# Optimization experiments

Hardware: AMD Instinct MI355X
Metric: run time of the kernel (lower is better)

The kernel has to match this reference:

```python
import jax, jax.numpy as jnp
import numpy as np

START_IDX = 1  # PAD_IDX = 0, END_IDX = 2 (unused in teacher-forcing path)
B, N, F = 16, 49, 1024
H, E, V = 1024, 1024, 15000
S, W = 5, 12


def setup_inputs() -> dict:
    key = jax.random.key(0)
    ks = jax.random.split(key, 16)
    def w(k, shape, s=0.02):
        return jax.random.normal(k, shape, dtype=jnp.float32) * s
    emb = w(ks[0], (V, E)).at[0].set(0.0)  # padding_idx = 0
    return dict(
        features=jax.random.normal(ks[1], (B, N, F), dtype=jnp.float32),
        reports=jax.random.randint(ks[2], (B, S, W), 0, V),
        attn_w1=w(ks[3], (F + H, H)), attn_b1=jnp.zeros((H,), jnp.float32),
        attn_w2=w(ks[4], (H, 1)), attn_b2=jnp.zeros((1,), jnp.float32),
        s_wih=w(ks[5], (4 * H, F)), s_whh=w(ks[6], (4 * H, H)),
        s_bih=jnp.zeros((4 * H,), jnp.float32), s_bhh=jnp.zeros((4 * H,), jnp.float32),
        stop_w=w(ks[7], (H, 1)), stop_b=jnp.zeros((1,), jnp.float32),
        emb=emb,
        w_wih=w(ks[8], (4 * H, E)), w_whh=w(ks[9], (4 * H, H)),
        w_bih=jnp.zeros((4 * H,), jnp.float32), w_bhh=jnp.zeros((4 * H,), jnp.float32),
        fc_w=w(ks[10], (H, V)), fc_b=jnp.zeros((V,), jnp.float32),
    )


def _lstm_cell(x, h, c, wih, whh, bih, bhh):
    # PyTorch LSTMCell: gates ordered i, f, g, o
    gates = x @ wih.T + h @ whh.T + (bih + bhh)
    i, f, g, o = jnp.split(gates, 4, axis=-1)
    c = jax.nn.sigmoid(f) * c + jax.nn.sigmoid(i) * jnp.tanh(g)
    h = jax.nn.sigmoid(o) * jnp.tanh(c)
    return h, c


def _attention(features, h, w1, b1, w2, b2):
    # features [B,N,F], h [B,H] -> additive 2-layer attention over N locations
    b, n, _ = features.shape
    hcat = jnp.broadcast_to(h[:, None, :], (b, n, h.shape[-1]))
    x = jnp.concatenate([features, hcat], axis=-1)           # [B,N,F+H]
    e = (jnp.tanh(x @ w1 + b1) @ w2 + b2)[..., 0]            # [B,N]
    scores = jax.nn.softmax(e, axis=-1)
    att = jnp.einsum('bn,bnf->bf', scores, features)          # [B,F]
    return att, scores


def _forward(features, reports, attn_w1, attn_b1, attn_w2, attn_b2,
             s_wih, s_whh, s_bih, s_bhh, stop_w, stop_b, emb,
             w_wih, w_whh, w_bih, w_bhh, fc_w, fc_b):
    bsz = features.shape[0]
    h0 = jnp.zeros((bsz, s_whh.shape[-1]), features.dtype)
    att0, _ = _attention(features, h0, attn_w1, attn_b1, attn_w2, attn_b2)
    start_emb = jnp.broadcast_to(emb[START_IDX][None, :], (bsz, emb.shape[-1]))

    def sentence_step(carry, reports_i):   # reports_i: [W, B] teacher-forcing tokens
        h, c, att = carry
        h, c = _lstm_cell(att, h, c, s_wih, s_whh, s_bih, s_bhh)
        czero = jnp.zeros_like(h)

        def word_step(wc, idx):
            hw, cw, inp = wc
            hw, cw = _lstm_cell(inp, hw, cw, w_wih, w_whh, w_bih, w_bhh)
            pred = hw @ fc_w + fc_b                           # [B,V]
            return (hw, cw, emb[idx]), pred

        # word LSTM initialized with h=topic, c=0; first input = <start> embedding
        _, preds = jax.lax.scan(word_step, (h, czero, start_emb), reports_i)  # [W,B,V]
        stop = jax.nn.sigmoid(h @ stop_w + stop_b)[:, 0]      # [B]
        att, scores = _attention(features, h, attn_w1, attn_b1, attn_w2, attn_b2)
        return (h, c, att), (preds, stop, scores)

    reports_sw = jnp.transpose(reports, (1, 2, 0))            # [S,W,B]
    _, (seq, stops, scores) = jax.lax.scan(sentence_step, (h0, h0, att0), reports_sw)
    seq_out = jnp.transpose(seq, (2, 0, 1, 3))                # [B,S,W,V]
    stops_out = jnp.transpose(stops, (1, 0))                  # [B,S]
    scores_out = jnp.transpose(scores, (1, 0, 2))             # [B,S,N]
    return seq_out, stops_out, scores_out


def reference(features, reports, attn_w1, attn_b1, attn_w2, attn_b2,
              s_wih, s_whh, s_bih, s_bhh, stop_w, stop_b, emb,
              w_wih, w_whh, w_bih, w_bhh, fc_w, fc_b):
    return _forward(features, reports, attn_w1, attn_b1, attn_w2, attn_b2,
                    s_wih, s_whh, s_bih, s_bhh, stop_w, stop_b, emb,
                    w_wih, w_whh, w_bih, w_bhh, fc_w, fc_b)
```

## Files before the change

kernel.cpp:

```cpp
#include <hip/hip_runtime.h>
#include <hip/hip_bf16.h>

#define B_  16
#define S_  5
#define W_  12
#define NL_ 49
#define H_  1024
#define V_  15000
#define SEQ_N   14400000
#define STOP_N  80
#define OUT_STOP (SEQ_N)
#define OUT_SCORE (SEQ_N + STOP_N)

typedef __attribute__((ext_vector_type(8))) short     short8;
typedef __attribute__((ext_vector_type(4))) float     f32x4;
typedef __attribute__((ext_vector_type(4))) unsigned int u32x4;
typedef __attribute__((ext_vector_type(4))) unsigned short us4;

#define OFF_FCWT   0ull
#define OFF_WWHHP  30720000ull
#define OFF_WWIHP  39108608ull
#define OFF_WSCATP 47497216ull
#define OFF_W1AT   64274432ull
#define OFF_W1BT   66371584ull
#define OFF_FBF    68468736ull
#define OFF_XIN    70074368ull
#define OFF_PF     72040448ull
#define OFF_XW     75251712ull
#define OFF_HBALL  90980352ull
#define OFF_HWBF0  92946432ull
#define OFF_HWBF1  93110272ull
#define OFF_ACAT1  93274112ull
#define OFF_H      93339648ull
#define OFF_EVAL   93405184ull
#define OFF_ACAT0  93408384ull
#define OFF_C      93473920ull
#define OFF_CW     93539456ull
#define OFF_HPROJ  93867136ull
#define WS_TOTAL   93932672ull
#define ZERO_BASE  OFF_ACAT0
#define ZERO_BYTES (524288ull)

__device__ __forceinline__ unsigned short f2bf(float x){
  unsigned u = __float_as_uint(x);
  u += 0x7fffu + ((u >> 16) & 1u);
  return (unsigned short)(u >> 16);
}
__device__ __forceinline__ float sigm(float x){ return 1.f/(1.f+expf(-x)); }

typedef __attribute__((address_space(3))) unsigned int  as3_u32;
typedef __attribute__((address_space(1))) const unsigned int as1_u32;

__device__ __forceinline__ void gl16(const void* g, void* l){
  __builtin_amdgcn_global_load_lds((as1_u32*)g, (as3_u32*)l, 16, 0, 0);
}

template<int ROWS,int CH,int NW>
__device__ __forceinline__ void stage_swz(const unsigned short* __restrict__ gbase, int grs,
                                          unsigned short* lds, int wid, int lane,
                                          int r0, int rmax){
  constexpr int RPI = 64/CH;
  constexpr int NISS = ROWS/RPI;
  const int r_in = lane / CH;
  const int cbp  = lane % CH;
  #pragma unroll
  for (int it = wid; it < NISS; it += NW){
    int rl = it*RPI + r_in;
    int gr = r0 + rl; gr = gr < rmax ? gr : rmax-1;
    int cb = cbp ^ (rl & 7);
    gl16(gbase + (size_t)gr*grs + cb*8, lds + it*RPI*CH*8);
  }
}

__device__ __forceinline__ void transp64(const float* __restrict__ src, int sld,
                                         int rb, int cb, int Cc,
                                         unsigned short* __restrict__ dst, int dld,
                                         float (*t)[65])
{
  const int tx = threadIdx.x & 15, ty = threadIdx.x >> 4;
  #pragma unroll
  for (int ii = 0; ii < 4; ii++){
    int r = ty + ii*16;
    int c = cb + tx*4;
    const float* s = src + (size_t)(rb + r)*sld + c;
    f32x4 v;
    if (c + 4 <= Cc) v = *(const f32x4*)s;
    else {
      v[0] = (c   < Cc) ? s[0] : 0.f;
      v[1] = (c+1 < Cc) ? s[1] : 0.f;
      v[2] = (c+2 < Cc) ? s[2] : 0.f;
      v[3] = (c+3 < Cc) ? s[3] : 0.f;
    }
    t[r][tx*4+0]=v[0]; t[r][tx*4+1]=v[1]; t[r][tx*4+2]=v[2]; t[r][tx*4+3]=v[3];
  }
  __syncthreads();
  #pragma unroll
  for (int ii = 0; ii < 4; ii++){
    int c = ty + ii*16;
    if (cb + c < Cc){
      int r4 = tx*4;
      us4 o; o[0]=f2bf(t[r4][c]); o[1]=f2bf(t[r4+1][c]); o[2]=f2bf(t[r4+2][c]); o[3]=f2bf(t[r4+3][c]);
      *(us4*)(dst + (size_t)(cb + c)*dld + rb + r4) = o;
    }
  }
}

#define U0 200704u
#define U1 (U0+1048576u)
#define U2 (U1+1048576u)
#define U3 (U2+1048576u)
#define U4 (U3+1048576u)
#define U5 (U4+245760u)
#define NCVT_BLK 1280
#define NTR_BLK  2136
#define NZ_BLK   16
#define NPREP    (NCVT_BLK + NTR_BLK + NZ_BLK)

__device__ __forceinline__ void cvt_gate_unit(const float* __restrict__ src,
                                              unsigned short* __restrict__ dst,
                                              unsigned e, int dld, int doff){
  int n = e >> 8, cc = (e & 255)*4;
  int gate = (n >> 4) & 3, j = ((n >> 6) << 4) | (n & 15);
  f32x4 v = *(const f32x4*)(src + ((size_t)(gate*1024 + j) << 10) + cc);
  us4 o; o[0]=f2bf(v[0]); o[1]=f2bf(v[1]); o[2]=f2bf(v[2]); o[3]=f2bf(v[3]);
  *(us4*)(dst + (size_t)n*dld + doff + cc) = o;
}

__global__ void k_prep(const float* __restrict__ features,
                       const float* __restrict__ w_whh, const float* __restrict__ w_wih,
                       const float* __restrict__ s_wih, const float* __restrict__ s_whh,
                       const float* __restrict__ emb, const int* __restrict__ reports,
                       const float* __restrict__ attn_w1, const float* __restrict__ fc_w,
                       unsigned short* __restrict__ FBF, unsigned short* __restrict__ WWHHP,
                       unsigned short* __restrict__ WWIHP, unsigned short* __restrict__ WSCATP,
                       unsigned short* __restrict__ XIN,
                       unsigned short* __restrict__ W1AT, unsigned short* __restrict__ W1BT,
                       unsigned short* __restrict__ FCWT, char* __restrict__ zbase)
{
  __shared__ float t[64][65];
  int bx = blockIdx.x;
  if (bx < NCVT_BLK){
    for (unsigned u = bx*256u + threadIdx.x; u < U5; u += NCVT_BLK*256u){
      if (u < U0){
        int idx = u*4;
        f32x4 v = *(const f32x4*)(features + idx);
        us4 o; o[0]=f2bf(v[0]); o[1]=f2bf(v[1]); o[2]=f2bf(v[2]); o[3]=f2bf(v[3]);
        *(us4*)(FBF + idx) = o;
      } else if (u < U1){
        cvt_gate_unit(w_whh, WWHHP, u - U0, 1024, 0);
      } else if (u < U2){
        cvt_gate_unit(w_wih, WWIHP, u - U1, 1024, 0);
      } else if (u < U3){
        cvt_gate_unit(s_wih, WSCATP, u - U2, 2048, 0);
      } else if (u < U4){
        cvt_gate_unit(s_whh, WSCATP, u - U3, 2048, 1024);
      } else {
        unsigned e = u - U4;
        int m = e >> 8, k = (e & 255)*4;
        int w = m / 80, r = m % 80, s = r >> 4, b = r & 15;
        int tok = (w == 0) ? 1 : reports[b*60 + s*12 + (w-1)];
        f32x4 v = *(const f32x4*)(emb + ((size_t)tok << 10) + k);
        us4 o; o[0]=f2bf(v[0]); o[1]=f2bf(v[1]); o[2]=f2bf(v[2]); o[3]=f2bf(v[3]);
        *(us4*)(XIN + (size_t)m*1024 + k) = o;
      }
    }
  } else if (bx < NCVT_BLK + NTR_BLK){
    int base = (bx - NCVT_BLK)*2;
    #pragma unroll
    for (int bt = 0; bt < 2; bt++){
      if (bt) __syncthreads();
      int tile = base + bt;
      if (tile < 512){
        int z = tile >> 8, rem = tile & 255;
        int rb = (rem & 15)*64, cb = (rem >> 4)*64;
        transp64(attn_w1 + (size_t)z*1024*1024, 1024, rb, cb, 1024, z ? W1BT : W1AT, 1024, t);
      } else {
        int ft = tile - 512;
        int rb = (ft & 15)*64, cb = (ft >> 4)*64;
        transp64(fc_w, V_, rb, cb, V_, FCWT, 1024, t);
      }
    }
  } else {
    int idx = bx - (NCVT_BLK + NTR_BLK);
    #pragma unroll
    for (int it = 0; it < 8; it++){
      size_t off = ((size_t)(idx + it*NZ_BLK))*4096 + threadIdx.x*16;
      *(u32x4*)(zbase + off) = (u32x4){0u,0u,0u,0u};
    }
  }
}

template<int BM,int BN,int BK,int WM,int WN,int EPI>
__device__ __forceinline__ void gemm_core(
    unsigned short* As, unsigned short* Bs,
    const unsigned short* __restrict__ A, int lda,
    const unsigned short* __restrict__ Bt, int ldb,
    float* __restrict__ C, int ldc,
    const float* __restrict__ bias,
    int M, int N, int K, int n0, int m0)
{
  constexpr int NWV = WM*WN;
  constexpr int CH = BK/8;
  const int tid  = threadIdx.x;
  const int lane = tid & 63;
  const int wave = tid >> 6;
  constexpr int WROWS = BM/WM, WCOLS = BN/WN;
  constexpr int FM = WROWS/16, FN = WCOLS/16;
  const int wm = wave / WN, wn = wave % WN;
  const int g = lane >> 4, fr = lane & 15;
  const int sx = fr & 7;

  f32x4 acc[FM][FN];
  #pragma unroll
  for (int a=0;a<FM;a++)
    #pragma unroll
    for (int b=0;b<FN;b++) acc[a][b] = (f32x4){0.f,0.f,0.f,0.f};

  for (int k0 = 0; k0 < K; k0 += BK) {
    if (k0) __syncthreads();
    stage_swz<BM,CH,NWV>(A + k0, lda, As, wave, lane, m0, M);
    stage_swz<BN,CH,NWV>(Bt + k0, ldb, Bs, wave, lane, n0, N);
    __syncthreads();
    #pragma unroll
    for (int kk = 0; kk < BK; kk += 32) {
      const int so = ((kk/8 + g) ^ sx) * 8;
      short8 af[FM], bt[FN];
      #pragma unroll
      for (int fm=0; fm<FM; fm++)
        af[fm] = *(const short8*)(As + (wm*WROWS + fm*16 + fr)*BK + so);
      #pragma unroll
      for (int fn=0; fn<FN; fn++)
        bt[fn] = *(const short8*)(Bs + (wn*WCOLS + fn*16 + fr)*BK + so);
      #pragma unroll
      for (int fm=0; fm<FM; fm++)
        #pragma unroll
        for (int fn=0; fn<FN; fn++)
          acc[fm][fn] = __builtin_amdgcn_mfma_f32_16x16x32_bf16(af[fm], bt[fn], acc[fm][fn], 0, 0, 0);
    }
  }

  #pragma unroll
  for (int fm=0; fm<FM; fm++)
    #pragma unroll
    for (int fn=0; fn<FN; fn++)
      #pragma unroll
      for (int j=0; j<4; j++){
        int m = m0 + wm*WROWS + fm*16 + g*4 + j;
        int n = n0 + wn*WCOLS + fn*16 + fr;
        if (m < M && n < N) {
          float v = acc[fm][fn][j];
          if (EPI == 1 || EPI == 2) v += bias[n];
          if (EPI == 2) {
            int b = m & 15, s = (m >> 4) % 5, w = m / 80;
            __builtin_nontemporal_store(v, &C[(size_t)((b*5 + s)*12 + w)*V_ + n]);
          } else if (EPI == 3) {
            __builtin_nontemporal_store(v, &C[(size_t)m*ldc + n]);
          } else {
            C[(size_t)m*ldc + n] = v;
          }
        }
      }
}

template<int BM,int BN,int BK,int WM,int WN,int EPI>
__global__ void k_gemm(const unsigned short* __restrict__ A, int lda,
                       const unsigned short* __restrict__ Bt, int ldb,
                       float* __restrict__ C, int ldc,
                       const float* __restrict__ bias,
                       int M, int N, int K)
{
  __shared__ __align__(16) unsigned short As[BM*BK];
  __shared__ __align__(16) unsigned short Bs[BN*BK];
  const int n0 = blockIdx.x * BN, m0 = blockIdx.y * BM;
  if (n0 >= N) return;
  gemm_core<BM,BN,BK,WM,WN,EPI>(As, Bs, A, lda, Bt, ldb, C, ldc, bias, M, N, K, n0, m0);
}

__global__ void __launch_bounds__(256) k_pf_xw(
    const unsigned short* __restrict__ FBF, const unsigned short* __restrict__ W1AT,
    float* __restrict__ PF, const float* __restrict__ attn_b1,
    const unsigned short* __restrict__ XIN, const unsigned short* __restrict__ WWIHP,
    float* __restrict__ XW)
{
  extern __shared__ __align__(16) unsigned short smem[];
  unsigned short* As = smem;
  unsigned short* Bs = smem + 64*128;
  int bx = blockIdx.x;
  if (bx < 208){
    int n0 = (bx & 15)*64, m0 = (bx >> 4)*64;
    gemm_core<64,64,128,2,2,1>(As, Bs, FBF,1024, W1AT,1024, PF,1024, attn_b1,
                               784,1024,1024, n0, m0);
  } else {
    int t = bx - 208;
    int n0 = (t & 31)*128, m0 = (t >> 5)*64;
    gemm_core<64,128,128,2,2,3>(As, Bs, XIN,1024, WWIHP,1024, XW,4096, nullptr,
                                960,4096,1024, n0, m0);
  }
}

template<int BM,int BN,int BK,int WN,int SENT>
__global__ void k_gemm_cell(const unsigned short* __restrict__ A, int lda,
                            const unsigned short* __restrict__ Bt, int ldb,
                            const float* __restrict__ Xg, int ldx,
                            const float* __restrict__ bih, const float* __restrict__ bhh,
                            float* __restrict__ cst,
                            unsigned short* __restrict__ h1, int ldh1,
                            unsigned short* __restrict__ h2,
                            float* __restrict__ hf,
                            int M, int K)
{
  constexpr int CH = BK/8;
  __shared__ __align__(16) unsigned short As[BM*BK];
  __shared__ __align__(16) unsigned short Bs[BN*BK];
  const int tid  = threadIdx.x;
  const int lane = tid & 63;
  const int wn   = tid >> 6;
  const int n0 = blockIdx.x * BN, m0 = blockIdx.y * BM;
  const int g = lane >> 4, fr = lane & 15;
  const int sx = fr & 7;

  f32x4 acc[4];
  #pragma unroll
  for (int b=0;b<4;b++) acc[b] = (f32x4){0.f,0.f,0.f,0.f};

  for (int k0 = 0; k0 < K; k0 += BK) {
    if (k0) __syncthreads();
    stage_swz<BM,CH,WN>(A + k0, lda, As, wn, lane, m0, M);
    stage_swz<BN,CH,WN>(Bt + k0, ldb, Bs, wn, lane, n0, 4096);
    __syncthreads();
    #pragma unroll
    for (int kk = 0; kk < BK; kk += 32) {
      const int so = ((kk/8 + g) ^ sx) * 8;
      short8 af = *(const short8*)(As + fr*BK + so);
      #pragma unroll
      for (int fn=0; fn<4; fn++){
        short8 bt = *(const short8*)(Bs + (wn*64 + fn*16 + fr)*BK + so);
        acc[fn] = __builtin_amdgcn_mfma_f32_16x16x32_bf16(af, bt, acc[fn], 0, 0, 0);
      }
    }
  }

  const int nb = n0 + wn*64 + fr;
  const int j  = ((n0 + wn*64) >> 2) + fr;
  const float b0 = bih[j]        + bhh[j];
  const float b1 = bih[1024 + j] + bhh[1024 + j];
  const float b2 = bih[2048 + j] + bhh[2048 + j];
  const float b3 = bih[3072 + j] + bhh[3072 + j];
  #pragma unroll
  for (int jj=0; jj<4; jj++){
    int m = m0 + g*4 + jj;
    if (m < M){
      float gi = acc[0][jj] + b0;
      float gf = acc[1][jj] + b1;
      float gg = acc[2][jj] + b2;
      float go = acc[3][jj] + b3;
      if (!SENT){
        const float* xg = Xg + (size_t)m*ldx + nb;
        gi += xg[0]; gf += xg[16]; gg += xg[32]; go += xg[48];
      }
      float cn = sigm(gf)*cst[m*1024 + j] + sigm(gi)*tanhf(gg);
      float hn = sigm(go)*tanhf(cn);
      cst[m*1024 + j] = cn;
      unsigned short hb = f2bf(hn);
      h1[(size_t)m*ldh1 + j] = hb;
      h2[(size_t)m*1024 + j] = hb;
      if (SENT) hf[m*1024 + j] = hn;
    }
  }
}

__global__ void k_attn_e(const float* __restrict__ PF, const float* __restrict__ hproj,
                         const float* __restrict__ w2, float* __restrict__ evals)
{
  const int bn = blockIdx.x;
  const int b  = bn / NL_;
  const int tid = threadIdx.x;
  __shared__ float red[4];
  const float* pf = PF + ((size_t)bn << 10);
  const float* hp = hproj + (b << 10);
  int k = tid * 4;
  f32x4 a = *(const f32x4*)(pf + k);
  f32x4 hh = *(const f32x4*)(hp + k);
  f32x4 w = *(const f32x4*)(w2 + k);
  float p = tanhf(a[0]+hh[0])*w[0] + tanhf(a[1]+hh[1])*w[1]
          + tanhf(a[2]+hh[2])*w[2] + tanhf(a[3]+hh[3])*w[3];
  #pragma unroll
  for (int o = 32; o; o >>= 1) p += __shfl_down(p, o, 64);
  if ((tid & 63) == 0) red[tid >> 6] = p;
  __syncthreads();
  if (tid == 0) evals[bn] = red[0] + red[1] + red[2] + red[3];
}

template<int INIT>
__global__ void k_attn_fin(const float* __restrict__ evals, const float* __restrict__ features,
                           const float* __restrict__ h, const float* __restrict__ stop_w,
                           const float* __restrict__ stop_b,
                           unsigned short* __restrict__ Acat, float* __restrict__ outp, int s)
{
  const int b = blockIdx.x, tid = threadIdx.x;
  __shared__ float scs[64];
  __shared__ float red[4];
  if (tid < 64){
    float e = (tid < NL_) ? evals[b*NL_ + tid] : -1e30f;
    float mx = e;
    #pragma unroll
    for (int o = 32; o; o >>= 1) mx = fmaxf(mx, __shfl_xor(mx, o, 64));
    float ex = (tid < NL_) ? expf(e - mx) : 0.f;
    float dn = ex;
    #pragma unroll
    for (int o = 32; o; o >>= 1) dn += __shfl_xor(dn, o, 64);
    float sc = ex / dn;
    if (tid < NL_){
      scs[tid] = sc;
      if (!INIT) outp[OUT_SCORE + (b*5 + s)*NL_ + tid] = sc;
    }
  }
  __syncthreads();
  {
    int f0 = tid * 4;
    f32x4 a = (f32x4){0.f,0.f,0.f,0.f};
    const float* fb = features + (((size_t)b*NL_) << 10) + f0;
    #pragma unroll 7
    for (int n = 0; n < NL_; n++){
      f32x4 v = *(const f32x4*)(fb + ((size_t)n << 10));
      float sc = scs[n];
      a[0] += sc*v[0]; a[1] += sc*v[1]; a[2] += sc*v[2]; a[3] += sc*v[3];
    }
    us4 o4; o4[0]=f2bf(a[0]); o4[1]=f2bf(a[1]); o4[2]=f2bf(a[2]); o4[3]=f2bf(a[3]);
    *(us4*)(Acat + b*2048 + f0) = o4;
  }
  if (!INIT){
    int k = tid * 4;
    f32x4 hv = *(const f32x4*)(h + (b << 10) + k);
    f32x4 sw = *(const f32x4*)(stop_w + k);
    float p = hv[0]*sw[0] + hv[1]*sw[1] + hv[2]*sw[2] + hv[3]*sw[3];
    #pragma unroll
    for (int o = 32; o; o >>= 1) p += __shfl_down(p, o, 64);
    if ((tid & 63) == 0) red[tid >> 6] = p;
    __syncthreads();
    if (tid == 0) outp[OUT_STOP + b*5 + s] = sigm(red[0]+red[1]+red[2]+red[3] + stop_b[0]);
  }
}

extern "C" void kernel_launch(void* const* d_in, const int* in_sizes, int n_in,
                              void* d_out, int out_size, void* d_ws, size_t ws_size,
                              hipStream_t stream)
{
  const float* features = (const float*)d_in[0];
  const int*   reports  = (const int*)d_in[1];
  const float* attn_w1  = (const float*)d_in[2];
  const float* attn_b1  = (const float*)d_in[3];
  const float* attn_w2  = (const float*)d_in[4];
  const float* s_wih    = (const float*)d_in[6];
  const float* s_whh    = (const float*)d_in[7];
  const float* s_bih    = (const float*)d_in[8];
  const float* s_bhh    = (const float*)d_in[9];
  const float* stop_w   = (const float*)d_in[10];
  const float* stop_b   = (const float*)d_in[11];
  const float* emb      = (const float*)d_in[12];
  const float* w_wih    = (const float*)d_in[13];
  const float* w_whh    = (const float*)d_in[14];
  const float* w_bih    = (const float*)d_in[15];
  const float* w_bhh    = (const float*)d_in[16];
  const float* fc_w     = (const float*)d_in[17];
  const float* fc_b     = (const float*)d_in[18];
  float* out = (float*)d_out;
  char*  ws  = (char*)d_ws;
  if (ws_size < WS_TOTAL) return;

  unsigned short* FCWT   = (unsigned short*)(ws + OFF_FCWT);
  unsigned short* WWHHP  = (unsigned short*)(ws + OFF_WWHHP);
  unsigned short* WWIHP  = (unsigned short*)(ws + OFF_WWIHP);
  unsigned short* WSCATP = (unsigned short*)(ws + OFF_WSCATP);
  unsigned short* W1AT   = (unsigned short*)(ws + OFF_W1AT);
  unsigned short* W1BT   = (unsigned short*)(ws + OFF_W1BT);
  unsigned short* FBF    = (unsigned short*)(ws + OFF_FBF);
  unsigned short* XIN    = (unsigned short*)(ws + OFF_XIN);
  float*          PF     = (float*)(ws + OFF_PF);
  float*          XW     = (float*)(ws + OFF_XW);
  unsigned short* HBALL  = (unsigned short*)(ws + OFF_HBALL);
  unsigned short* HW0    = (unsigned short*)(ws + OFF_HWBF0);
  unsigned short* HW1    = (unsigned short*)(ws + OFF_HWBF1);
  unsigned short* ACAT0  = (unsigned short*)(ws + OFF_ACAT0);
  unsigned short* ACAT1  = (unsigned short*)(ws + OFF_ACAT1);
  float*          Hst    = (float*)(ws + OFF_H);
  float*          Cst    = (float*)(ws + OFF_C);
  float*          CW     = (float*)(ws + OFF_CW);
  float*          HPROJ  = (float*)(ws + OFF_HPROJ);
  float*          EVAL   = (float*)(ws + OFF_EVAL);

  k_prep<<<NPREP, 256, 0, stream>>>(features, w_whh, w_wih, s_wih, s_whh, emb, reports,
                                    attn_w1, fc_w,
                                    FBF, WWHHP, WWIHP, WSCATP, XIN, W1AT, W1BT, FCWT,
                                    ws + ZERO_BASE);

  k_pf_xw<<<688, 256, 49152, stream>>>(FBF, W1AT, PF, attn_b1, XIN, WWIHP, XW);

  k_attn_e<<<784, 256, 0, stream>>>(PF, HPROJ, attn_w2, EVAL);
  k_attn_fin<1><<<16, 256, 0, stream>>>(EVAL, features, Hst, stop_w, stop_b, ACAT0, out, 0);

  unsigned short* ACS[2] = {ACAT0, ACAT1};
  for (int s = 0; s < S_; s++){
    unsigned short* cur = ACS[s & 1];
    unsigned short* nxt = ACS[(s + 1) & 1];
    k_gemm_cell<16,128,256,2,1><<<dim3(32,1), 128, 0, stream>>>(
        cur, 2048, WSCATP, 2048, nullptr, 0, s_bih, s_bhh, Cst,
        nxt + 1024, 2048, HW0 + s*16*1024, Hst, 16, 2048);
    k_gemm<16,64,256,1,4,0><<<dim3(16,1), 256, 0, stream>>>(
        nxt + 1024, 2048, W1BT, 1024, HPROJ, 1024, nullptr, 16, 1024, 1024);
    k_attn_e<<<784, 256, 0, stream>>>(PF, HPROJ, attn_w2, EVAL);
    k_attn_fin<0><<<16, 256, 0, stream>>>(EVAL, features, Hst, stop_w, stop_b, nxt, out, s);
  }

  unsigned short* HW[2] = {HW0, HW1};
  for (int w = 0; w < W_; w++){
    k_gemm_cell<16,128,256,2,0><<<dim3(32,5), 128, 0, stream>>>(
        HW[w & 1], 1024, WWHHP, 1024, XW + (size_t)w*80*4096, 4096, w_bih, w_bhh, CW,
        HW[(w + 1) & 1], 1024, HBALL + (size_t)w*80*1024, nullptr, 80, 1024);
  }

  k_gemm<64,128,64,2,2,2><<<dim3(120,15), 256, 0, stream>>>(HBALL,1024, FCWT,1024, out,V_, fc_b, 960,15000,1024);
}
```

Baseline: 504.0 us.

## Fuse word-LSTM time steps into one persistent kernel with grid barrier

Replaces twelve separate per-step word-LSTM GEMM+cell launches with a single persistent kernel of 160 blocks that loops over time steps and synchronizes through a global atomic counter barrier in workspace. The barrier memory is zeroed by the prep kernel. This is meant to remove per-launch overhead and inter-kernel gaps along the serial recurrence. It relies on all 160 blocks being co-resident and adds spin-wait latency on each step.

Result: slower. 621.7 us (+23.4%).

```diff
diff --git a/kernel.cpp b/kernel.cpp
--- a/kernel.cpp
+++ b/kernel.cpp
@@ -37,9 +37,9 @@
 #define OFF_C      93473920ull
 #define OFF_CW     93539456ull
 #define OFF_HPROJ  93867136ull
-#define WS_TOTAL   93932672ull
+#define OFF_BAR    93932672ull
+#define WS_TOTAL   93936768ull
 #define ZERO_BASE  OFF_ACAT0
-#define ZERO_BYTES (524288ull)
 
 __device__ __forceinline__ unsigned short f2bf(float x){
   unsigned u = __float_as_uint(x);
@@ -187,6 +187,8 @@
       size_t off = ((size_t)(idx + it*NZ_BLK))*4096 + threadIdx.x*16;
       *(u32x4*)(zbase + off) = (u32x4){0u,0u,0u,0u};
     }
+    if (idx == 0)
+      *(u32x4*)(zbase + 524288 + threadIdx.x*16) = (u32x4){0u,0u,0u,0u};
   }
 }
 
@@ -365,6 +367,87 @@
       h1[(size_t)m*ldh1 + j] = hb;
       h2[(size_t)m*1024 + j] = hb;
       if (SENT) hf[m*1024 + j] = hn;
+    }
+  }
+}
+
+__global__ void __launch_bounds__(128) k_word_chain(
+    const unsigned short* __restrict__ Bt,
+    const float* __restrict__ XW,
+    const float* __restrict__ bih, const float* __restrict__ bhh,
+    float* __restrict__ cw,
+    unsigned short* __restrict__ HW0, unsigned short* __restrict__ HW1,
+    unsigned short* __restrict__ Hball,
+    unsigned* __restrict__ bar)
+{
+  constexpr int BK = 256, CH = BK/8;
+  __shared__ __align__(16) unsigned short As[16*BK];
+  __shared__ __align__(16) unsigned short Bs[128*BK];
+  const int tid = threadIdx.x, lane = tid & 63, wn = tid >> 6;
+  const int n0 = blockIdx.x * 128, m0 = blockIdx.y * 16;
+  const int g = lane >> 4, fr = lane & 15, sx = fr & 7;
+
+  const int nb = n0 + wn*64 + fr;
+  const int j  = ((n0 + wn*64) >> 2) + fr;
+  const float b0 = bih[j]        + bhh[j];
+  const float b1 = bih[1024 + j] + bhh[1024 + j];
+  const float b2 = bih[2048 + j] + bhh[2048 + j];
+  const float b3 = bih[3072 + j] + bhh[3072 + j];
+  unsigned short* HW[2] = {HW0, HW1};
+
+  for (int w = 0; w < W_; w++){
+    const unsigned short* A = HW[w & 1];
+    f32x4 acc[4];
+    #pragma unroll
+    for (int b=0;b<4;b++) acc[b] = (f32x4){0.f,0.f,0.f,0.f};
+    for (int k0 = 0; k0 < 1024; k0 += BK){
+      if (k0) __syncthreads();
+      stage_swz<16,CH,2>(A + k0, 1024, As, wn, lane, m0, 80);
+      stage_swz<128,CH,2>(Bt + k0, 1024, Bs, wn, lane, n0, 4096);
+      __syncthreads();
+      #pragma unroll
+      for (int kk = 0; kk < BK; kk += 32){
+        const int so = ((kk/8 + g) ^ sx) * 8;
+        short8 af = *(const short8*)(As + fr*BK + so);
+        #pragma unroll
+        for (int fn=0; fn<4; fn++){
+          short8 bt = *(const short8*)(Bs + (wn*64 + fn*16 + fr)*BK + so);
+          acc[fn] = __builtin_amdgcn_mfma_f32_16x16x32_bf16(af, bt, acc[fn], 0, 0, 0);
+        }
+      }
+    }
+    unsigned short* hnext = HW[(w + 1) & 1];
+    unsigned short* hb_out = Hball + (size_t)w*80*1024;
+    const float* xgb = XW + (size_t)(w*80)*4096;
+    #pragma unroll
+    for (int jj=0; jj<4; jj++){
+      int m = m0 + g*4 + jj;
+      const float* xg = xgb + (size_t)m*4096 + nb;
+      float gi = acc[0][jj] + b0 + xg[0];
+      float gf = acc[1][jj] + b1 + xg[16];
+      float gg = acc[2][jj] + b2 + xg[32];
+      float go = acc[3][jj] + b3 + xg[48];
+      float cn = sigm(gf)*cw[m*1024 + j] + sigm(gi)*tanhf(gg);
+      float hn = sigm(go)*tanhf(cn);
+      cw[m*1024 + j] = cn;
+      unsigned short hb = f2bf(hn);
+      hnext[(size_t)m*1024 + j] = hb;
+      hb_out[(size_t)m*1024 + j] = hb;
+    }
+    if (w < W_ - 1){
+      __syncthreads();
+      if (tid == 0){
+        __threadfence();
+        unsigned old = atomicAdd(&bar[0], 1u);
+        if (old == 160u*(unsigned)(w + 1) - 1u){
+          __hip_atomic_store(&bar[1], (unsigned)(w + 1), __ATOMIC_RELEASE, __HIP_MEMORY_SCOPE_AGENT);
+        } else {
+          while (__hip_atomic_load(&bar[1], __ATOMIC_ACQUIRE, __HIP_MEMORY_SCOPE_AGENT) < (unsigned)(w + 1))
+            __builtin_amdgcn_s_sleep(2);
+        }
+        __threadfence();
+      }
+      __syncthreads();
     }
   }
 }
@@ -488,6 +571,7 @@
   float*          CW     = (float*)(ws + OFF_CW);
   float*          HPROJ  = (float*)(ws + OFF_HPROJ);
   float*          EVAL   = (float*)(ws + OFF_EVAL);
+  unsigned*       BAR    = (unsigned*)(ws + OFF_BAR);
 
   k_prep<<<NPREP, 256, 0, stream>>>(features, w_whh, w_wih, s_wih, s_whh, emb, reports,
                                     attn_w1, fc_w,
@@ -512,12 +596,7 @@
     k_attn_fin<0><<<16, 256, 0, stream>>>(EVAL, features, Hst, stop_w, stop_b, nxt, out, s);
   }
 
-  unsigned short* HW[2] = {HW0, HW1};
-  for (int w = 0; w < W_; w++){
-    k_gemm_cell<16,128,256,2,0><<<dim3(32,5), 128, 0, stream>>>(
-        HW[w & 1], 1024, WWHHP, 1024, XW + (size_t)w*80*4096, 4096, w_bih, w_bhh, CW,
-        HW[(w + 1) & 1], 1024, HBALL + (size_t)w*80*1024, nullptr, 80, 1024);
-  }
+  k_word_chain<<<dim3(32,5), 128, 0, stream>>>(WWHHP, XW, w_bih, w_bhh, CW, HW0, HW1, HBALL, BAR);
 
   k_gemm<64,128,64,2,2,2><<<dim3(120,15), 256, 0, stream>>>(HBALL,1024, FCWT,1024, out,V_, fc_b, 960,15000,1024);
 }
```
